# Kernel optimization log

Hardware: AMD Instinct MI355X
Metric: run time of the kernel (lower is better)

The kernel has to match this reference:

```python
import jax, jax.numpy as jnp
import numpy as np
import math

B, Q, K, C, H, D = 2, 2048, 2048, 512, 8, 64  # hidden_dim*num_heads == C


def setup_inputs() -> dict:
    key = jax.random.key(0)
    ks = jax.random.split(key, 9)
    s = 0.02
    return {
        "query_data": jax.random.normal(ks[0], (B, Q, C), jnp.float32),
        "key_data": jax.random.normal(ks[1], (B, K, C), jnp.float32),
        "bias1": jax.random.normal(ks[2], (B, 1, Q, K), jnp.float32),
        "bias2": jax.random.normal(ks[3], (1, H, Q, K), jnp.float32),
        "wq": jax.random.normal(ks[4], (C, H * D), jnp.float32) * s,
        "wk": jax.random.normal(ks[5], (C, H * D), jnp.float32) * s,
        "wv": jax.random.normal(ks[6], (C, H * D), jnp.float32) * s,
        "wo": jax.random.normal(ks[7], (H * D, C), jnp.float32) * s,
        "bo": jnp.zeros((C,), jnp.float32),
        "wg": jax.random.normal(ks[8], (C, H * D), jnp.float32) * s,
        "bg": jnp.zeros((H * D,), jnp.float32),
    }


def reference(query_data, key_data, bias1, bias2, wq, wk, wv, wo, bo, wg, bg):
    # prep_qkv: project, split heads, scale q by 1/sqrt(hidden_dim)
    q = (query_data @ wq).reshape(B, Q, H, D) / math.sqrt(D)
    k = (key_data @ wk).reshape(B, K, H, D)
    v = (key_data @ wv).reshape(B, K, H, D)
    # attention: scores [B,H,Q,K] with additive biases, softmax over K
    scores = jnp.einsum("bqhd,bkhd->bhqk", q, k) + bias1 + bias2
    attn = jax.nn.softmax(scores, axis=-1)
    out = jnp.einsum("bhqk,bkhd->bqhd", attn, v)  # [B,Q,H,D]
    # wrap_up: sigmoid gate from query data, flatten heads, output proj
    g = jax.nn.sigmoid(query_data @ wg + bg).reshape(B, Q, H, D)
    out = (out * g).reshape(B, Q, H * D)
    return out @ wo + bo
```

## Files before the change

### kernel.cpp

```cpp
#include <hip/hip_runtime.h>

typedef __bf16 bf16;
typedef __bf16 bf16x8 __attribute__((ext_vector_type(8)));
typedef __bf16 bf16x4 __attribute__((ext_vector_type(4)));
typedef float f32x4 __attribute__((ext_vector_type(4)));

#define NB 2
#define NQ 2048
#define NKK 2048
#define NC 512
#define NH 8
#define ND 64
#define NM (NB*NQ)
#define SPLITS 4
#define KSPL (NKK/SPLITS)
#define NTILES (KSPL/32)
#define PLS 36

__global__ __launch_bounds__(256) void cvt_bf16_kernel(const float* __restrict__ in,
                                                       bf16* __restrict__ out, int n4) {
  int i = blockIdx.x * 256 + threadIdx.x;
  if (i < n4) {
    float4 v = ((const float4*)in)[i];
    bf16x4 o;
    o[0] = (bf16)v.x; o[1] = (bf16)v.y; o[2] = (bf16)v.z; o[3] = (bf16)v.w;
    ((bf16x4*)out)[i] = o;
  }
}

__global__ __launch_bounds__(256) void transpose_w_kernel(const float* __restrict__ W,
                                                          bf16* __restrict__ WT) {
  __shared__ float t[32][33];
  int n0 = blockIdx.x * 32, k0 = blockIdx.y * 32;
  int c = threadIdx.x & 31, r0 = threadIdx.x >> 5;
  for (int r = r0; r < 32; r += 8) t[r][c] = W[(size_t)(k0 + r) * NC + n0 + c];
  __syncthreads();
  for (int r = r0; r < 32; r += 8) WT[(size_t)(n0 + r) * NC + k0 + c] = (bf16)t[c][r];
}

__global__ __launch_bounds__(256) void gemm_kernel(const bf16* __restrict__ X,
                                                   const bf16* __restrict__ WT,
                                                   const float* __restrict__ bias,
                                                   void* __restrict__ out, int epi) {
  __shared__ bf16 Xs[64][72];
  __shared__ bf16 Ws[64][72];
  int m0 = blockIdx.y * 64, n0 = blockIdx.x * 64;
  int tid = threadIdx.x, lane = tid & 63, wave = tid >> 6;
  int wm = wave >> 1, wn = wave & 1;
  int lr = lane & 15, lg = lane >> 4;
  f32x4 acc[2][2] = {};
  for (int k0 = 0; k0 < 512; k0 += 64) {
#pragma unroll
    for (int j = 0; j < 2; j++) {
      int cc = tid + 256 * j;
      int r = cc >> 3, c8 = (cc & 7) * 8;
      *(uint4*)&Xs[r][c8] = *(const uint4*)&X[(size_t)(m0 + r) * 512 + k0 + c8];
      *(uint4*)&Ws[r][c8] = *(const uint4*)&WT[(size_t)(n0 + r) * 512 + k0 + c8];
    }
    __syncthreads();
#pragma unroll
    for (int kk = 0; kk < 64; kk += 32) {
      bf16x8 a[2], b[2];
      a[0] = *(const bf16x8*)&Xs[wm * 32 + lr][kk + lg * 8];
      a[1] = *(const bf16x8*)&Xs[wm * 32 + 16 + lr][kk + lg * 8];
      b[0] = *(const bf16x8*)&Ws[wn * 32 + lr][kk + lg * 8];
      b[1] = *(const bf16x8*)&Ws[wn * 32 + 16 + lr][kk + lg * 8];
#pragma unroll
      for (int mi = 0; mi < 2; mi++)
#pragma unroll
        for (int ni = 0; ni < 2; ni++)
          acc[mi][ni] = __builtin_amdgcn_mfma_f32_16x16x32_bf16(a[mi], b[ni], acc[mi][ni], 0, 0, 0);
    }
    __syncthreads();
  }
#pragma unroll
  for (int mi = 0; mi < 2; mi++) {
#pragma unroll
    for (int ni = 0; ni < 2; ni++) {
#pragma unroll
      for (int i = 0; i < 4; i++) {
        int grow = m0 + wm * 32 + mi * 16 + lg * 4 + i;
        int gcol = n0 + wn * 32 + ni * 16 + lr;
        float v = acc[mi][ni][i];
        if (epi == 0) {
          int b = grow >> 11, q = grow & 2047, h = gcol >> 6, d = gcol & 63;
          ((bf16*)out)[((size_t)(b * NH + h) * NQ + q) * ND + d] = (bf16)(v * 0.125f);
        } else if (epi == 1 || epi == 2) {
          int b = grow >> 11, kq = grow & 2047, h = gcol >> 6, d = gcol & 63;
          ((bf16*)out)[((size_t)(b * NH + h) * NKK + kq) * ND + d] = (bf16)v;
        } else if (epi == 3) {
          v += bias[gcol];
          v = 1.0f / (1.0f + __expf(-v));
          ((float*)out)[(size_t)grow * 512 + gcol] = v;
        } else {
          ((float*)out)[(size_t)grow * 512 + gcol] = v + bias[gcol];
        }
      }
    }
  }
}

__global__ __launch_bounds__(256) void transpose_v_kernel(const bf16* __restrict__ vh,
                                                          bf16* __restrict__ vT) {
  __shared__ bf16 t[64][72];
  int bh = blockIdx.y;
  int kk0 = blockIdx.x * 64;
  const bf16* src = vh + (size_t)bh * NKK * ND;
  bf16* dst = vT + (size_t)bh * ND * NKK;
#pragma unroll
  for (int j = 0; j < 2; j++) {
    int c = threadIdx.x + 256 * j;
    int r = c >> 3, cc = (c & 7) * 8;
    *(uint4*)&t[r][cc] = *(const uint4*)&src[(size_t)(kk0 + r) * ND + cc];
  }
  __syncthreads();
#pragma unroll
  for (int j = 0; j < 2; j++) {
    int c = threadIdx.x + 256 * j;
    int d = c >> 3, ck = (c & 7) * 8;
    bf16 tmp[8];
#pragma unroll
    for (int x = 0; x < 8; x++) tmp[x] = t[ck + x][d];
    *(uint4*)&dst[(size_t)d * NKK + kk0 + ck] = *(const uint4*)tmp;
  }
}

__device__ __forceinline__ void gload16(const float* g, float* l) {
  __builtin_amdgcn_global_load_lds((const __attribute__((address_space(1))) void*)g,
                                   (__attribute__((address_space(3))) void*)l, 16, 0, 0);
}
__device__ __forceinline__ void gload4(const float* g, float* l) {
  __builtin_amdgcn_global_load_lds((const __attribute__((address_space(1))) void*)g,
                                   (__attribute__((address_space(3))) void*)l, 4, 0, 0);
}

__global__ __launch_bounds__(512, 4) void attn_kernel(
    const bf16* __restrict__ qh, const bf16* __restrict__ kh, const bf16* __restrict__ vT,
    const float* __restrict__ bias1, const float* __restrict__ bias2,
    float* __restrict__ o_part, float* __restrict__ l_part) {
  __shared__ float b1s[2][16 * 32];
  __shared__ float b2s[2][8 * 16 * 32];
  __shared__ bf16 plds[8][16][PLS];
  int l = blockIdx.x;
  int idx = (l & 7) * 128 + (l >> 3);
  int q0 = (idx & 127) * 16;
  int r = idx >> 7;
  int b = r & 1, split = r >> 1;
  int tid = threadIdx.x;
  int h = tid >> 6, lane = tid & 63;
  int lr = lane & 15, lg = lane >> 4;
  int kbase = split * KSPL;
  const bf16* Qp = qh + ((size_t)(b * NH + h) * NQ + q0) * ND;
  const bf16* Kp = kh + (size_t)(b * NH + h) * NKK * ND;
  const bf16* Vt = vT + (size_t)(b * NH + h) * ND * NKK;

  bf16x8 qf0 = *(const bf16x8*)&Qp[lr * 64 + lg * 8];
  bf16x8 qf1 = *(const bf16x8*)&Qp[lr * 64 + 32 + lg * 8];

  f32x4 o[4] = {};
  float lrow[4] = {0.f, 0.f, 0.f, 0.f};
  bf16(*pl)[PLS] = plds[h];

#define STAGE(c, s)                                                              \
  do {                                                                           \
    int kcol = kbase + (c) * 32;                                                 \
    _Pragma("unroll")                                                            \
    for (int j = 0; j < 2; j++) {                                                \
      int uu = tid + j * 512;                                                    \
      int h_ = uu >> 7, row_ = (uu >> 3) & 15, c4 = (uu & 7) * 4;                \
      gload16(bias2 + ((size_t)h_ * NQ + q0 + row_) * NKK + kcol + c4,           \
              &b2s[s][uu * 4]);                                                  \
    }                                                                            \
    int row1 = tid >> 5, col1 = tid & 31;                                        \
    gload4(bias1 + ((size_t)b * NQ + q0 + row1) * NKK + kcol + col1,             \
           &b1s[s][tid]);                                                        \
  } while (0)

  STAGE(0, 0);
  __syncthreads();

  for (int t = 0; t < NTILES; t++) {
    int s = t & 1;
    if (t + 1 < NTILES) STAGE(t + 1, s ^ 1);
    int k0 = kbase + t * 32;
    bf16x8 vf0 = *(const bf16x8*)&Vt[(size_t)(0 * 16 + lr) * NKK + k0 + lg * 8];
    bf16x8 vf1 = *(const bf16x8*)&Vt[(size_t)(1 * 16 + lr) * NKK + k0 + lg * 8];
    bf16x8 vf2 = *(const bf16x8*)&Vt[(size_t)(2 * 16 + lr) * NKK + k0 + lg * 8];
    bf16x8 vf3 = *(const bf16x8*)&Vt[(size_t)(3 * 16 + lr) * NKK + k0 + lg * 8];
    f32x4 sv[2];
#pragma unroll
    for (int f = 0; f < 2; f++) {
      const bf16* kp = Kp + (size_t)(k0 + f * 16 + lr) * ND + lg * 8;
      bf16x8 kfa = *(const bf16x8*)kp;
      bf16x8 kfb = *(const bf16x8*)(kp + 32);
      f32x4 c;
#pragma unroll
      for (int i = 0; i < 4; i++) {
        int off = (lg * 4 + i) * 32 + f * 16 + lr;
        c[i] = b1s[s][off] + b2s[s][h * 512 + off];
      }
      c = __builtin_amdgcn_mfma_f32_16x16x32_bf16(qf0, kfa, c, 0, 0, 0);
      c = __builtin_amdgcn_mfma_f32_16x16x32_bf16(qf1, kfb, c, 0, 0, 0);
      sv[f] = c;
    }
#pragma unroll
    for (int i = 0; i < 4; i++) {
      float p0 = __expf(sv[0][i]);
      float p1 = __expf(sv[1][i]);
      lrow[i] += p0 + p1;
      pl[lg * 4 + i][lr] = (bf16)p0;
      pl[lg * 4 + i][16 + lr] = (bf16)p1;
    }
    bf16x8 pa = *(const bf16x8*)&pl[lr][lg * 8];
    o[0] = __builtin_amdgcn_mfma_f32_16x16x32_bf16(pa, vf0, o[0], 0, 0, 0);
    o[1] = __builtin_amdgcn_mfma_f32_16x16x32_bf16(pa, vf1, o[1], 0, 0, 0);
    o[2] = __builtin_amdgcn_mfma_f32_16x16x32_bf16(pa, vf2, o[2], 0, 0, 0);
    o[3] = __builtin_amdgcn_mfma_f32_16x16x32_bf16(pa, vf3, o[3], 0, 0, 0);
    __syncthreads();
  }
#undef STAGE

  float lred[4];
#pragma unroll
  for (int i = 0; i < 4; i++) {
    float L = lrow[i];
    L += __shfl_xor(L, 1);
    L += __shfl_xor(L, 2);
    L += __shfl_xor(L, 4);
    L += __shfl_xor(L, 8);
    lred[i] = L;
  }

  float* op = o_part + (((size_t)(split * NB + b) * NH + h) * NQ + q0) * ND;
#pragma unroll
  for (int ni = 0; ni < 4; ni++)
#pragma unroll
    for (int i = 0; i < 4; i++)
      op[(lg * 4 + i) * ND + ni * 16 + lr] = o[ni][i];
  if (lr == 0) {
    float* lp = l_part + ((size_t)(split * NB + b) * NH + h) * NQ + q0;
#pragma unroll
    for (int i = 0; i < 4; i++) lp[lg * 4 + i] = lred[i];
  }
}

__global__ __launch_bounds__(256) void combine_kernel(const float* __restrict__ o_part,
                                                      const float* __restrict__ l_part,
                                                      const float* __restrict__ gate,
                                                      bf16* __restrict__ ao) {
  size_t t = (size_t)blockIdx.x * 256 + threadIdx.x;
  int d0 = (int)(t & 15) * 4;
  int h = (int)((t >> 4) & 7);
  int q = (int)((t >> 7) & 2047);
  int b = (int)(t >> 18);
  f32x4 acc = {};
  float L = 0.f;
#pragma unroll
  for (int s = 0; s < SPLITS; s++) {
    size_t base = (((size_t)(s * NB + b) * NH + h) * NQ + q);
    acc += *(const f32x4*)&o_part[base * ND + d0];
    L += l_part[base];
  }
  float inv = 1.0f / L;
  size_t gi = ((size_t)b * NQ + q) * 512 + h * 64 + d0;
  f32x4 g = *(const f32x4*)&gate[gi];
  bf16x4 r;
#pragma unroll
  for (int j = 0; j < 4; j++) r[j] = (bf16)(acc[j] * inv * g[j]);
  *(bf16x4*)&ao[gi] = r;
}

extern "C" void kernel_launch(void* const* d_in, const int* in_sizes, int n_in,
                              void* d_out, int out_size, void* d_ws, size_t ws_size,
                              hipStream_t stream) {
  const float* query = (const float*)d_in[0];
  const float* keyd  = (const float*)d_in[1];
  const float* bias1 = (const float*)d_in[2];
  const float* bias2 = (const float*)d_in[3];
  const float* wq = (const float*)d_in[4];
  const float* wk = (const float*)d_in[5];
  const float* wv = (const float*)d_in[6];
  const float* wo = (const float*)d_in[7];
  const float* bo = (const float*)d_in[8];
  const float* wg = (const float*)d_in[9];
  const float* bg = (const float*)d_in[10];

  char* ws = (char*)d_ws;
  size_t off = 0;
  auto alloc = [&](size_t bytes) {
    void* p = ws + off;
    off += (bytes + 255) & ~(size_t)255;
    return p;
  };
  bf16* qd_bf = (bf16*)alloc((size_t)NM * 512 * 2);
  bf16* kd_bf = (bf16*)alloc((size_t)NM * 512 * 2);
  bf16* wqT = (bf16*)alloc((size_t)512 * 512 * 2);
  bf16* wkT = (bf16*)alloc((size_t)512 * 512 * 2);
  bf16* wvT = (bf16*)alloc((size_t)512 * 512 * 2);
  bf16* wgT = (bf16*)alloc((size_t)512 * 512 * 2);
  bf16* woT = (bf16*)alloc((size_t)512 * 512 * 2);
  bf16* qh  = (bf16*)alloc((size_t)NB * NH * NQ * ND * 2);
  bf16* kh  = (bf16*)alloc((size_t)NB * NH * NKK * ND * 2);
  bf16* vh  = (bf16*)alloc((size_t)NB * NH * NKK * ND * 2);
  bf16* vTt = (bf16*)alloc((size_t)NB * NH * ND * NKK * 2);
  float* gbuf = (float*)alloc((size_t)NM * 512 * 4);
  bf16* aob = (bf16*)alloc((size_t)NM * 512 * 2);
  float* o_part = (float*)alloc((size_t)SPLITS * NB * NH * NQ * ND * 4);
  float* l_part = (float*)alloc((size_t)SPLITS * NB * NH * NQ * 4);

  int n4 = NM * 512 / 4;
  cvt_bf16_kernel<<<dim3(n4 / 256), 256, 0, stream>>>(query, qd_bf, n4);
  cvt_bf16_kernel<<<dim3(n4 / 256), 256, 0, stream>>>(keyd, kd_bf, n4);

  transpose_w_kernel<<<dim3(16, 16), 256, 0, stream>>>(wq, wqT);
  transpose_w_kernel<<<dim3(16, 16), 256, 0, stream>>>(wk, wkT);
  transpose_w_kernel<<<dim3(16, 16), 256, 0, stream>>>(wv, wvT);
  transpose_w_kernel<<<dim3(16, 16), 256, 0, stream>>>(wg, wgT);
  transpose_w_kernel<<<dim3(16, 16), 256, 0, stream>>>(wo, woT);

  gemm_kernel<<<dim3(8, 64), 256, 0, stream>>>(qd_bf, wqT, nullptr, qh, 0);
  gemm_kernel<<<dim3(8, 64), 256, 0, stream>>>(kd_bf, wkT, nullptr, kh, 1);
  gemm_kernel<<<dim3(8, 64), 256, 0, stream>>>(kd_bf, wvT, nullptr, vh, 2);
  gemm_kernel<<<dim3(8, 64), 256, 0, stream>>>(qd_bf, wgT, bg, gbuf, 3);

  transpose_v_kernel<<<dim3(32, 16), 256, 0, stream>>>(vh, vTt);

  attn_kernel<<<dim3(1024), 512, 0, stream>>>(qh, kh, vTt, bias1, bias2, o_part, l_part);

  combine_kernel<<<dim3((NB * NQ * NH * 16) / 256), 256, 0, stream>>>(o_part, l_part, gbuf, aob);

  gemm_kernel<<<dim3(8, 64), 256, 0, stream>>>(aob, woT, bo, d_out, 4);
}
```

Before: 253.0 us.

## Triple-buffer bias staging and register-prefetch K/V one tile ahead in attention

Moves the bias LDS staging from double to triple buffering and prefetches the K and V fragments for the next tile into a second register set, ping-ponging between the two sets across an unrolled-by-two loop. The full __syncthreads is replaced by a partial vmcnt wait plus s_barrier, so the in-flight loads for the next tile need not drain before computing the current one. The goal is to hide global and bias load latency behind the MFMA and exp work. In exchange it adds LDS use and register pressure, which could lower occupancy under the 512x4 launch bounds. It also relies on a hand-counted vmcnt value being correct.

Result: slower. 408.2 us (+61.3%).

```diff
diff --git a/kernel.cpp b/kernel.cpp
--- a/kernel.cpp
+++ b/kernel.cpp
@@ -138,8 +138,8 @@
     const bf16* __restrict__ qh, const bf16* __restrict__ kh, const bf16* __restrict__ vT,
     const float* __restrict__ bias1, const float* __restrict__ bias2,
     float* __restrict__ o_part, float* __restrict__ l_part) {
-  __shared__ float b1s[2][16 * 32];
-  __shared__ float b2s[2][8 * 16 * 32];
+  __shared__ float b1s[3][16 * 32];
+  __shared__ float b2s[3][8 * 16 * 32];
   __shared__ bf16 plds[8][16][PLS];
   int l = blockIdx.x;
   int idx = (l & 7) * 128 + (l >> 3);
@@ -151,8 +151,8 @@
   int lr = lane & 15, lg = lane >> 4;
   int kbase = split * KSPL;
   const bf16* Qp = qh + ((size_t)(b * NH + h) * NQ + q0) * ND;
-  const bf16* Kp = kh + (size_t)(b * NH + h) * NKK * ND;
-  const bf16* Vt = vT + (size_t)(b * NH + h) * ND * NKK;
+  const bf16* Kp = kh + (size_t)(b * NH + h) * NKK * ND + (size_t)kbase * ND;
+  const bf16* Vt = vT + (size_t)(b * NH + h) * ND * NKK + kbase;
 
   bf16x8 qf0 = *(const bf16x8*)&Qp[lr * 64 + lg * 8];
   bf16x8 qf1 = *(const bf16x8*)&Qp[lr * 64 + 32 + lg * 8];
@@ -161,7 +161,7 @@
   float lrow[4] = {0.f, 0.f, 0.f, 0.f};
   bf16(*pl)[PLS] = plds[h];
 
-#define STAGE(c, s)                                                              \
+#define STAGE(c, slot)                                                           \
   do {                                                                           \
     int kcol = kbase + (c) * 32;                                                 \
     _Pragma("unroll")                                                            \
@@ -169,56 +169,95 @@
       int uu = tid + j * 512;                                                    \
       int h_ = uu >> 7, row_ = (uu >> 3) & 15, c4 = (uu & 7) * 4;                \
       gload16(bias2 + ((size_t)h_ * NQ + q0 + row_) * NKK + kcol + c4,           \
-              &b2s[s][uu * 4]);                                                  \
+              &b2s[slot][uu * 4]);                                               \
     }                                                                            \
     int row1 = tid >> 5, col1 = tid & 31;                                        \
     gload4(bias1 + ((size_t)b * NQ + q0 + row1) * NKK + kcol + col1,             \
-           &b1s[s][tid]);                                                        \
+           &b1s[slot][tid]);                                                     \
   } while (0)
 
+#define LOADKV(c, K0, K1, K2, K3, V0, V1, V2, V3)                                \
+  do {                                                                           \
+    const bf16* kp = Kp + (size_t)((c) * 32 + lr) * ND + lg * 8;                 \
+    K0 = *(const bf16x8*)kp;                                                     \
+    K1 = *(const bf16x8*)(kp + 32);                                              \
+    K2 = *(const bf16x8*)(kp + 16 * ND);                                         \
+    K3 = *(const bf16x8*)(kp + 16 * ND + 32);                                    \
+    V0 = *(const bf16x8*)&Vt[(size_t)(0 * 16 + lr) * NKK + (c) * 32 + lg * 8];   \
+    V1 = *(const bf16x8*)&Vt[(size_t)(1 * 16 + lr) * NKK + (c) * 32 + lg * 8];   \
+    V2 = *(const bf16x8*)&Vt[(size_t)(2 * 16 + lr) * NKK + (c) * 32 + lg * 8];   \
+    V3 = *(const bf16x8*)&Vt[(size_t)(3 * 16 + lr) * NKK + (c) * 32 + lg * 8];   \
+  } while (0)
+
+#define WAIT_BARRIER()                                                           \
+  do {                                                                           \
+    asm volatile("s_waitcnt vmcnt(11)" ::: "memory");                            \
+    __builtin_amdgcn_s_barrier();                                                \
+    asm volatile("" ::: "memory");                                               \
+  } while (0)
+
+#define COMPUTE(slot, K0, K1, K2, K3, V0, V1, V2, V3)                            \
+  do {                                                                           \
+    f32x4 sv0, sv1;                                                              \
+    {                                                                            \
+      f32x4 c;                                                                   \
+      _Pragma("unroll")                                                          \
+      for (int i = 0; i < 4; i++) {                                              \
+        int off = (lg * 4 + i) * 32 + lr;                                        \
+        c[i] = b1s[slot][off] + b2s[slot][h * 512 + off];                        \
+      }                                                                          \
+      c = __builtin_amdgcn_mfma_f32_16x16x32_bf16(qf0, K0, c, 0, 0, 0);          \
+      c = __builtin_amdgcn_mfma_f32_16x16x32_bf16(qf1, K1, c, 0, 0, 0);          \
+      sv0 = c;                                                                   \
+    }                                                                            \
+    {                                                                            \
+      f32x4 c;                                                                   \
+      _Pragma("unroll")                                                          \
+      for (int i = 0; i < 4; i++) {                                              \
+        int off = (lg * 4 + i) * 32 + 16 + lr;                                   \
+        c[i] = b1s[slot][off] + b2s[slot][h * 512 + off];                        \
+      }                                                                          \
+      c = __builtin_amdgcn_mfma_f32_16x16x32_bf16(qf0, K2, c, 0, 0, 0);          \
+      c = __builtin_amdgcn_mfma_f32_16x16x32_bf16(qf1, K3, c, 0, 0, 0);          \
+      sv1 = c;                                                                   \
+    }                                                                            \
+    _Pragma("unroll")                                                            \
+    for (int i = 0; i < 4; i++) {                                                \
+      float p0 = __expf(sv0[i]);                                                 \
+      float p1 = __expf(sv1[i]);                                                 \
+      lrow[i] += p0 + p1;                                                        \
+      pl[lg * 4 + i][lr] = (bf16)p0;                                             \
+      pl[lg * 4 + i][16 + lr] = (bf16)p1;                                        \
+    }                                                                            \
+    bf16x8 pa = *(const bf16x8*)&pl[lr][lg * 8];                                 \
+    o[0] = __builtin_amdgcn_mfma_f32_16x16x32_bf16(pa, V0, o[0], 0, 0, 0);       \
+    o[1] = __builtin_amdgcn_mfma_f32_16x16x32_bf16(pa, V1, o[1], 0, 0, 0);       \
+    o[2] = __builtin_amdgcn_mfma_f32_16x16x32_bf16(pa, V2, o[2], 0, 0, 0);       \
+    o[3] = __builtin_amdgcn_mfma_f32_16x16x32_bf16(pa, V3, o[3], 0, 0, 0);       \
+  } while (0)
+
+  bf16x8 kA0, kA1, kA2, kA3, vA0, vA1, vA2, vA3;
+  bf16x8 kB0, kB1, kB2, kB3, vB0, vB1, vB2, vB3;
+
   STAGE(0, 0);
-  __syncthreads();
-
-  for (int t = 0; t < NTILES; t++) {
-    int s = t & 1;
-    if (t + 1 < NTILES) STAGE(t + 1, s ^ 1);
-    int k0 = kbase + t * 32;
-    bf16x8 vf0 = *(const bf16x8*)&Vt[(size_t)(0 * 16 + lr) * NKK + k0 + lg * 8];
-    bf16x8 vf1 = *(const bf16x8*)&Vt[(size_t)(1 * 16 + lr) * NKK + k0 + lg * 8];
-    bf16x8 vf2 = *(const bf16x8*)&Vt[(size_t)(2 * 16 + lr) * NKK + k0 + lg * 8];
-    bf16x8 vf3 = *(const bf16x8*)&Vt[(size_t)(3 * 16 + lr) * NKK + k0 + lg * 8];
-    f32x4 sv[2];
-#pragma unroll
-    for (int f = 0; f < 2; f++) {
-      const bf16* kp = Kp + (size_t)(k0 + f * 16 + lr) * ND + lg * 8;
-      bf16x8 kfa = *(const bf16x8*)kp;
-      bf16x8 kfb = *(const bf16x8*)(kp + 32);
-      f32x4 c;
-#pragma unroll
-      for (int i = 0; i < 4; i++) {
-        int off = (lg * 4 + i) * 32 + f * 16 + lr;
-        c[i] = b1s[s][off] + b2s[s][h * 512 + off];
-      }
-      c = __builtin_amdgcn_mfma_f32_16x16x32_bf16(qf0, kfa, c, 0, 0, 0);
-      c = __builtin_amdgcn_mfma_f32_16x16x32_bf16(qf1, kfb, c, 0, 0, 0);
-      sv[f] = c;
-    }
-#pragma unroll
-    for (int i = 0; i < 4; i++) {
-      float p0 = __expf(sv[0][i]);
-      float p1 = __expf(sv[1][i]);
-      lrow[i] += p0 + p1;
-      pl[lg * 4 + i][lr] = (bf16)p0;
-      pl[lg * 4 + i][16 + lr] = (bf16)p1;
-    }
-    bf16x8 pa = *(const bf16x8*)&pl[lr][lg * 8];
-    o[0] = __builtin_amdgcn_mfma_f32_16x16x32_bf16(pa, vf0, o[0], 0, 0, 0);
-    o[1] = __builtin_amdgcn_mfma_f32_16x16x32_bf16(pa, vf1, o[1], 0, 0, 0);
-    o[2] = __builtin_amdgcn_mfma_f32_16x16x32_bf16(pa, vf2, o[2], 0, 0, 0);
-    o[3] = __builtin_amdgcn_mfma_f32_16x16x32_bf16(pa, vf3, o[3], 0, 0, 0);
-    __syncthreads();
+  LOADKV(0, kA0, kA1, kA2, kA3, vA0, vA1, vA2, vA3);
+
+  for (int t = 0; t < NTILES; t += 2) {
+    int n1 = (t + 1 < NTILES) ? t + 1 : NTILES - 1;
+    int n2 = (t + 2 < NTILES) ? t + 2 : NTILES - 1;
+    STAGE(n1, (t + 1) % 3);
+    LOADKV(n1, kB0, kB1, kB2, kB3, vB0, vB1, vB2, vB3);
+    WAIT_BARRIER();
+    COMPUTE(t % 3, kA0, kA1, kA2, kA3, vA0, vA1, vA2, vA3);
+    STAGE(n2, (t + 2) % 3);
+    LOADKV(n2, kA0, kA1, kA2, kA3, vA0, vA1, vA2, vA3);
+    WAIT_BARRIER();
+    COMPUTE((t + 1) % 3, kB0, kB1, kB2, kB3, vB0, vB1, vB2, vB3);
   }
 #undef STAGE
+#undef LOADKV
+#undef WAIT_BARRIER
+#undef COMPUTE
 
   float lred[4];
 #pragma unroll
```

## Stage attention biases in 16-column chunks with finer pipelining and higher occupancy

Applied to the files above, without the earlier changes.

The attention kernel now stages bias tiles in 16-key chunks instead of 32, halving shared memory per block. It processes two sub-chunks per loop iteration with a barrier between them, overlapping the next bias load with score computation. The launch bound is raised to 8 blocks per CU to exploit the smaller LDS footprint. This may cause register pressure or spills and adds one extra barrier per 32 keys.

Result: slower. 307.3 us (+21.4%).

```diff
diff --git a/kernel.cpp b/kernel.cpp
--- a/kernel.cpp
+++ b/kernel.cpp
@@ -14,7 +14,8 @@
 #define NM (NB*NQ)
 #define SPLITS 4
 #define KSPL (NKK/SPLITS)
-#define NTILES (KSPL/32)
+#define CHK 16
+#define NCH (KSPL/CHK)
 #define PLS 36
 
 __global__ __launch_bounds__(256) void cvt_bf16_kernel(const float* __restrict__ in,
@@ -134,12 +135,12 @@
                                    (__attribute__((address_space(3))) void*)l, 4, 0, 0);
 }
 
-__global__ __launch_bounds__(512, 4) void attn_kernel(
+__global__ __launch_bounds__(512, 8) void attn_kernel(
     const bf16* __restrict__ qh, const bf16* __restrict__ kh, const bf16* __restrict__ vT,
     const float* __restrict__ bias1, const float* __restrict__ bias2,
     float* __restrict__ o_part, float* __restrict__ l_part) {
-  __shared__ float b1s[2][16 * 32];
-  __shared__ float b2s[2][8 * 16 * 32];
+  __shared__ float b1s[2][16 * 16];
+  __shared__ float b2s[2][8 * 16 * 16];
   __shared__ bf16 plds[8][16][PLS];
   int l = blockIdx.x;
   int idx = (l & 7) * 128 + (l >> 3);
@@ -151,8 +152,8 @@
   int lr = lane & 15, lg = lane >> 4;
   int kbase = split * KSPL;
   const bf16* Qp = qh + ((size_t)(b * NH + h) * NQ + q0) * ND;
-  const bf16* Kp = kh + (size_t)(b * NH + h) * NKK * ND;
-  const bf16* Vt = vT + (size_t)(b * NH + h) * ND * NKK;
+  const bf16* Kp = kh + (size_t)(b * NH + h) * NKK * ND + (size_t)kbase * ND;
+  const bf16* Vt = vT + (size_t)(b * NH + h) * ND * NKK + kbase;
 
   bf16x8 qf0 = *(const bf16x8*)&Qp[lr * 64 + lg * 8];
   bf16x8 qf1 = *(const bf16x8*)&Qp[lr * 64 + 32 + lg * 8];
@@ -161,64 +162,62 @@
   float lrow[4] = {0.f, 0.f, 0.f, 0.f};
   bf16(*pl)[PLS] = plds[h];
 
-#define STAGE(c, s)                                                              \
-  do {                                                                           \
-    int kcol = kbase + (c) * 32;                                                 \
-    _Pragma("unroll")                                                            \
-    for (int j = 0; j < 2; j++) {                                                \
-      int uu = tid + j * 512;                                                    \
-      int h_ = uu >> 7, row_ = (uu >> 3) & 15, c4 = (uu & 7) * 4;                \
-      gload16(bias2 + ((size_t)h_ * NQ + q0 + row_) * NKK + kcol + c4,           \
-              &b2s[s][uu * 4]);                                                  \
-    }                                                                            \
-    int row1 = tid >> 5, col1 = tid & 31;                                        \
-    gload4(bias1 + ((size_t)b * NQ + q0 + row1) * NKK + kcol + col1,             \
-           &b1s[s][tid]);                                                        \
+  const float* b2src = bias2 + ((size_t)(tid >> 6) * NQ + q0 + ((tid & 63) >> 2)) * NKK +
+                       kbase + (tid & 3) * 4;
+  const float* b1src = bias1 + ((size_t)b * NQ + q0 + (tid >> 4)) * NKK + kbase + (tid & 15);
+
+#define STAGE(c, s)                                   \
+  do {                                                \
+    gload16(b2src + (c) * CHK, &b2s[s][tid * 4]);     \
+    if (tid < 256) gload4(b1src + (c) * CHK, &b1s[s][tid]); \
+  } while (0)
+
+#define SUBCHUNK(t, s, pc)                                                     \
+  do {                                                                         \
+    int k0 = (t) * CHK;                                                        \
+    bf16x8 kf0 = *(const bf16x8*)&Kp[(size_t)(k0 + lr) * ND + lg * 8];         \
+    bf16x8 kf1 = *(const bf16x8*)&Kp[(size_t)(k0 + lr) * ND + 32 + lg * 8];    \
+    f32x4 c;                                                                   \
+    _Pragma("unroll")                                                          \
+    for (int i = 0; i < 4; i++) {                                              \
+      int off = (lg * 4 + i) * 16 + lr;                                        \
+      c[i] = b1s[s][off] + b2s[s][h * 256 + off];                              \
+    }                                                                          \
+    c = __builtin_amdgcn_mfma_f32_16x16x32_bf16(qf0, kf0, c, 0, 0, 0);         \
+    c = __builtin_amdgcn_mfma_f32_16x16x32_bf16(qf1, kf1, c, 0, 0, 0);         \
+    _Pragma("unroll")                                                          \
+    for (int i = 0; i < 4; i++) {                                              \
+      float p = __expf(c[i]);                                                  \
+      lrow[i] += p;                                                            \
+      pl[lg * 4 + i][(pc) + lr] = (bf16)p;                                     \
+    }                                                                          \
   } while (0)
 
   STAGE(0, 0);
   __syncthreads();
 
-  for (int t = 0; t < NTILES; t++) {
-    int s = t & 1;
-    if (t + 1 < NTILES) STAGE(t + 1, s ^ 1);
-    int k0 = kbase + t * 32;
-    bf16x8 vf0 = *(const bf16x8*)&Vt[(size_t)(0 * 16 + lr) * NKK + k0 + lg * 8];
-    bf16x8 vf1 = *(const bf16x8*)&Vt[(size_t)(1 * 16 + lr) * NKK + k0 + lg * 8];
-    bf16x8 vf2 = *(const bf16x8*)&Vt[(size_t)(2 * 16 + lr) * NKK + k0 + lg * 8];
-    bf16x8 vf3 = *(const bf16x8*)&Vt[(size_t)(3 * 16 + lr) * NKK + k0 + lg * 8];
-    f32x4 sv[2];
-#pragma unroll
-    for (int f = 0; f < 2; f++) {
-      const bf16* kp = Kp + (size_t)(k0 + f * 16 + lr) * ND + lg * 8;
-      bf16x8 kfa = *(const bf16x8*)kp;
-      bf16x8 kfb = *(const bf16x8*)(kp + 32);
-      f32x4 c;
-#pragma unroll
-      for (int i = 0; i < 4; i++) {
-        int off = (lg * 4 + i) * 32 + f * 16 + lr;
-        c[i] = b1s[s][off] + b2s[s][h * 512 + off];
-      }
-      c = __builtin_amdgcn_mfma_f32_16x16x32_bf16(qf0, kfa, c, 0, 0, 0);
-      c = __builtin_amdgcn_mfma_f32_16x16x32_bf16(qf1, kfb, c, 0, 0, 0);
-      sv[f] = c;
+  for (int t = 0; t < NCH; t += 2) {
+    STAGE(t + 1, 1);
+    SUBCHUNK(t, 0, 0);
+    __syncthreads();
+    if (t + 2 < NCH) STAGE(t + 2, 0);
+    SUBCHUNK(t + 1, 1, 16);
+    {
+      int kv0 = t * CHK;
+      bf16x8 vf0 = *(const bf16x8*)&Vt[(size_t)(0 * 16 + lr) * NKK + kv0 + lg * 8];
+      bf16x8 vf1 = *(const bf16x8*)&Vt[(size_t)(1 * 16 + lr) * NKK + kv0 + lg * 8];
+      bf16x8 vf2 = *(const bf16x8*)&Vt[(size_t)(2 * 16 + lr) * NKK + kv0 + lg * 8];
+      bf16x8 vf3 = *(const bf16x8*)&Vt[(size_t)(3 * 16 + lr) * NKK + kv0 + lg * 8];
+      bf16x8 pa = *(const bf16x8*)&pl[lr][lg * 8];
+      o[0] = __builtin_amdgcn_mfma_f32_16x16x32_bf16(pa, vf0, o[0], 0, 0, 0);
+      o[1] = __builtin_amdgcn_mfma_f32_16x16x32_bf16(pa, vf1, o[1], 0, 0, 0);
+      o[2] = __builtin_amdgcn_mfma_f32_16x16x32_bf16(pa, vf2, o[2], 0, 0, 0);
+      o[3] = __builtin_amdgcn_mfma_f32_16x16x32_bf16(pa, vf3, o[3], 0, 0, 0);
     }
-#pragma unroll
-    for (int i = 0; i < 4; i++) {
-      float p0 = __expf(sv[0][i]);
-      float p1 = __expf(sv[1][i]);
-      lrow[i] += p0 + p1;
-      pl[lg * 4 + i][lr] = (bf16)p0;
-      pl[lg * 4 + i][16 + lr] = (bf16)p1;
-    }
-    bf16x8 pa = *(const bf16x8*)&pl[lr][lg * 8];
-    o[0] = __builtin_amdgcn_mfma_f32_16x16x32_bf16(pa, vf0, o[0], 0, 0, 0);
-    o[1] = __builtin_amdgcn_mfma_f32_16x16x32_bf16(pa, vf1, o[1], 0, 0, 0);
-    o[2] = __builtin_amdgcn_mfma_f32_16x16x32_bf16(pa, vf2, o[2], 0, 0, 0);
-    o[3] = __builtin_amdgcn_mfma_f32_16x16x32_bf16(pa, vf3, o[3], 0, 0, 0);
     __syncthreads();
   }
 #undef STAGE
+#undef SUBCHUNK
 
   float lred[4];
 #pragma unroll
```
